# Kernel tuning notes

Measured on AMD Instinct MI355X. Metric: run time of the kernel, lower is better.

Reference implementation:

```python
import jax, jax.numpy as jnp
import numpy as np
from jax import lax

B, L, T = 16, 128, 1024          # batch, phoneme len, mel frames
D, H, F, NL = 384, 2, 1536, 6    # d_model, heads, ffn dim, layers per stack
V, NMEL, CDP = 128, 80, 256      # vocab, mel bins, duration-predictor channels
NEG = -1e9

def make_posenc(max_pos, d):
    pos = np.arange(max_pos, dtype=np.float32)[:, None]
    i = np.arange(d, dtype=np.float32)[None, :]
    ang = pos / np.power(10000.0, 2.0 * np.floor(i / 2.0) / d)
    pe = np.zeros((max_pos, d), np.float32)
    pe[:, 0::2] = np.sin(ang[:, 0::2])
    pe[:, 1::2] = np.cos(ang[:, 1::2])
    return jnp.asarray(pe)

POS = make_posenc(T, D)

def layer_norm(x, g, b, eps=1e-6):
    m = jnp.mean(x, -1, keepdims=True)
    v = jnp.mean(jnp.square(x - m), -1, keepdims=True)
    return (x - m) * lax.rsqrt(v + eps) * g + b

def mha(x, wq, bq, wk, bk, wv, bv, wo, bo, mask):
    b, s, d = x.shape
    dh = d // H
    def split(t):
        return t.reshape(b, s, H, dh).transpose(0, 2, 1, 3)  # bhsd
    q, k, v = split(x @ wq + bq), split(x @ wk + bk), split(x @ wv + bv)
    logits = jnp.einsum('bhqd,bhkd->bhqk', q, k) / jnp.sqrt(jnp.float32(dh))
    logits = logits + mask * NEG  # mask: [B,1,1,S], 1.0 = masked (as in source)
    w = jax.nn.softmax(logits, axis=-1)
    o = jnp.einsum('bhqk,bhkd->bhqd', w, v).transpose(0, 2, 1, 3).reshape(b, s, d)
    return o @ wo + bo

def fft_stack(x, mask, aw, ab, w1, b1, w2, b2, lnp):
    for i in range(aw.shape[0]):
        a = mha(x, aw[i, 0], ab[i, 0], aw[i, 1], ab[i, 1], aw[i, 2], ab[i, 2], aw[i, 3], ab[i, 3], mask)
        x = layer_norm(x + a, lnp[i, 0, 0], lnp[i, 0, 1])
        f = jax.nn.relu(x @ w1[i] + b1[i]) @ w2[i] + b2[i]
        x = layer_norm(x + f, lnp[i, 1, 0], lnp[i, 1, 1])
    return x

def conv1d_same(x, w, b):
    # x: [B,S,Cin], w: [K,Cin,Cout]
    return lax.conv_general_dilated(x, w, (1,), 'SAME', dimension_numbers=('NWC', 'WIO', 'NWC')) + b

def setup_inputs() -> dict:
    key = jax.random.key(0)
    ks = iter(jax.random.split(key, 24))
    nrm = lambda shape: jax.random.normal(next(ks), shape, jnp.float32) * 0.02
    ln_init = lambda nl, c: jnp.broadcast_to(jnp.stack([jnp.ones(c, jnp.float32), jnp.zeros(c, jnp.float32)]), (nl, 2, 2, c))
    inp = {
        'phonemes': jax.random.randint(next(ks), (B, L), 1, V, jnp.int32),
        'durations': jax.random.randint(next(ks), (B, L), 1, 16, jnp.int32),
        'embed': nrm((V, D)),
        'alpha_enc': jnp.float32(1.0),
        'alpha_dec': jnp.float32(1.0),
        'enc_attn_w': nrm((NL, 4, D, D)), 'enc_attn_b': jnp.zeros((NL, 4, D), jnp.float32),
        'enc_ffn_w1': nrm((NL, D, F)), 'enc_ffn_b1': jnp.zeros((NL, F), jnp.float32),
        'enc_ffn_w2': nrm((NL, F, D)), 'enc_ffn_b2': jnp.zeros((NL, D), jnp.float32),
        'enc_ln': ln_init(NL, D),
        'dec_attn_w': nrm((NL, 4, D, D)), 'dec_attn_b': jnp.zeros((NL, 4, D), jnp.float32),
        'dec_ffn_w1': nrm((NL, D, F)), 'dec_ffn_b1': jnp.zeros((NL, F), jnp.float32),
        'dec_ffn_w2': nrm((NL, F, D)), 'dec_ffn_b2': jnp.zeros((NL, D), jnp.float32),
        'dec_ln': ln_init(NL, D),
        'dp_conv1_w': nrm((3, D, CDP)), 'dp_conv1_b': jnp.zeros((CDP,), jnp.float32),
        'dp_conv2_w': nrm((3, CDP, CDP)), 'dp_conv2_b': jnp.zeros((CDP,), jnp.float32),
        'dp_ln': jnp.broadcast_to(jnp.stack([jnp.ones(CDP, jnp.float32), jnp.zeros(CDP, jnp.float32)]), (2, 2, CDP)),
        'dp_out_w': nrm((CDP, 1)), 'dp_out_b': jnp.zeros((1,), jnp.float32),
        'mel_w': nrm((D, NMEL)), 'mel_b': jnp.zeros((NMEL,), jnp.float32),
    }
    return inp

def reference(phonemes, durations, embed, alpha_enc, alpha_dec,
              enc_attn_w, enc_attn_b, enc_ffn_w1, enc_ffn_b1, enc_ffn_w2, enc_ffn_b2, enc_ln,
              dec_attn_w, dec_attn_b, dec_ffn_w1, dec_ffn_b1, dec_ffn_w2, dec_ffn_b2, dec_ln,
              dp_conv1_w, dp_conv1_b, dp_conv2_w, dp_conv2_b, dp_ln, dp_out_w, dp_out_b,
              mel_w, mel_b):
    Lp = phonemes.shape[1]
    # phoneme encoder with scaled positional encoding
    x = embed[phonemes] + alpha_enc * POS[None, :Lp, :]
    enc_mask = (phonemes == 0).astype(jnp.float32)[:, None, None, :]
    h = fft_stack(x, enc_mask, enc_attn_w, enc_attn_b, enc_ffn_w1, enc_ffn_b1, enc_ffn_w2, enc_ffn_b2, enc_ln)
    # duration predictor: conv1d -> relu -> LN, x2, then linear (log durations)
    d1 = layer_norm(jax.nn.relu(conv1d_same(h, dp_conv1_w, dp_conv1_b)), dp_ln[0, 0], dp_ln[0, 1])
    d2 = layer_norm(jax.nn.relu(conv1d_same(d1, dp_conv2_w, dp_conv2_b)), dp_ln[1, 0], dp_ln[1, 1])
    dur_pred = (d2 @ dp_out_w + dp_out_b)[..., 0]  # [B, L]
    # length regulator: expand each phoneme state by its (teacher) duration via gather
    cum = jnp.cumsum(durations, axis=1)  # [B, L]
    frames = jnp.arange(T)
    idx = jax.vmap(lambda c: jnp.searchsorted(c, frames, side='right'))(cum)  # [B, T]
    idx = jnp.clip(idx, 0, Lp - 1)
    y = jnp.take_along_axis(h, idx[:, :, None], axis=1)  # [B, T, D]
    valid = (frames[None, :] < cum[:, -1:]).astype(jnp.float32)  # [B, T]
    y = y * valid[:, :, None]
    # mel decoder
    y = y + alpha_dec * POS[None, :T, :]
    dec_mask = (1.0 - valid)[:, None, None, :]
    m = fft_stack(y, dec_mask, dec_attn_w, dec_attn_b, dec_ffn_w1, dec_ffn_b1, dec_ffn_w2, dec_ffn_b2, dec_ln)
    mel = m @ mel_w + mel_b  # [B, T, NMEL]
    return mel, dur_pred
```

## Files before the change

### kernel.cpp

```cpp
#include <hip/hip_runtime.h>
#include <math.h>

#define BATCH 16
#define LPH 128
#define TFR 1024
#define DMODEL 384
#define FDIM 1536
#define NLAYER 6
#define NMELB 80
#define CDPC 256
#define NEGV (-1e9f)

typedef unsigned short u16;
typedef __attribute__((ext_vector_type(8))) short short8;
typedef __attribute__((ext_vector_type(4))) float f32x4;

__device__ __forceinline__ float b2f(u16 u) {
  return __uint_as_float(((unsigned)u) << 16);
}
__device__ __forceinline__ u16 f2b(float f) {
  unsigned x = __float_as_uint(f);
  return (u16)((x + 0x7fffu + ((x >> 16) & 1u)) >> 16);
}
__device__ __forceinline__ unsigned cvtpk(float lo, float hi) {
  unsigned r;
  asm volatile("v_cvt_pk_bf16_f32 %0, %1, %2" : "=v"(r) : "v"(lo), "v"(hi));
  return r;
}

#define GLOAD16(gp, lp)                                                                   \
  __builtin_amdgcn_global_load_lds((const __attribute__((address_space(1))) void*)(gp),   \
                                   (__attribute__((address_space(3))) void*)(lp), 16, 0, 0)

#define FBIAS 1
#define FRES 2
#define FRELU 4
#define FOB16 8
#define FVT 16

template <int FL>
__global__ __launch_bounds__(256) void bgemm(
    const u16* __restrict__ A, const u16* __restrict__ Bt,
    const float* __restrict__ bias, const float* __restrict__ res,
    void* __restrict__ Cv, u16* __restrict__ VtP,
    int N, int K, int lda, int ldb, int ldc,
    int zdiv, long az0, long az1, long bz0, long bz1, long cz0, long cz1, int S) {
  constexpr int SMEMSZ = (FL & FVT) ? (128 * 136) : 8192;
  __shared__ __align__(16) u16 smem[SMEMSZ];
  u16* As = smem;
  u16* Bs = smem + 4096;
  const int tid = threadIdx.x;
  const int wave = tid >> 6, lane = tid & 63;
  const int wm = wave >> 1, wn = wave & 1;
  const int lrow = lane & 15, lk = lane >> 4;
  const int z = blockIdx.z;
  const int zq = z / zdiv, zr = z - zq * zdiv;
  const long offA = (long)zq * az0 + (long)zr * az1;
  const long offB = (long)zq * bz0 + (long)zr * bz1;
  const long offC = (long)zq * cz0 + (long)zr * cz1;
  const int fid = blockIdx.x + gridDim.x * blockIdx.y;
  const int idx = fid >> 3;
  const int xl = idx % gridDim.x;
  const int yl = (fid & 7) + 8 * (idx / gridDim.x);
  const int row0 = yl * 128;
  const int col0 = xl * 128;

  const int sj = wave * 2;
  const int srow = lane >> 2;
  const int skc = (lane & 3) * 8;
  const u16* gA = A + offA + (long)(row0 + sj * 16 + srow) * lda + skc;
  const u16* gB = Bt + offB + (long)(col0 + sj * 16 + srow) * ldb + skc;
  u16* lA = As + sj * 512;
  u16* lB = Bs + sj * 512;
  const long ldak = 16L * lda;
  const long ldbk = 16L * ldb;

  f32x4 acc[4][4];
  const f32x4 zero4 = {0.f, 0.f, 0.f, 0.f};
#pragma unroll
  for (int i = 0; i < 4; i++)
#pragma unroll
    for (int j = 0; j < 4; j++) acc[i][j] = zero4;

  const int aoff = (wm * 64 + lrow) * 32 + lk * 8;
  const int boff = (wn * 64 + lrow) * 32 + lk * 8;

  for (int k0 = 0; k0 < K; k0 += 32) {
    GLOAD16(gA, lA);
    GLOAD16(gA + ldak, lA + 512);
    GLOAD16(gB, lB);
    GLOAD16(gB + ldbk, lB + 512);
    gA += 32; gB += 32;
    __syncthreads();
    short8 av[4], bv[4];
#pragma unroll
    for (int mi = 0; mi < 4; mi++) av[mi] = *(const short8*)&As[aoff + mi * 512];
#pragma unroll
    for (int ni = 0; ni < 4; ni++) bv[ni] = *(const short8*)&Bs[boff + ni * 512];
#pragma unroll
    for (int mi = 0; mi < 4; mi++)
#pragma unroll
      for (int ni = 0; ni < 4; ni++)
        acc[mi][ni] = __builtin_amdgcn_mfma_f32_16x16x32_bf16(av[mi], bv[ni], acc[mi][ni], 0, 0, 0);
    __syncthreads();
  }

  const float* bz = (FL & FBIAS) ? bias + (long)z * N : nullptr;
  if constexpr ((FL & FVT) != 0) {
    if (z == 2) {
      u16* Ts = smem;
#pragma unroll
      for (int mi = 0; mi < 4; mi++) {
        int si = wm * 64 + lk * 4 + mi * 16;
#pragma unroll
        for (int ni = 0; ni < 4; ni++) {
          int cl = wn * 64 + ni * 16 + lrow;
          float bi = bz[col0 + cl];
          ushort4 o;
          o.x = f2b(acc[mi][ni][0] + bi);
          o.y = f2b(acc[mi][ni][1] + bi);
          o.z = f2b(acc[mi][ni][2] + bi);
          o.w = f2b(acc[mi][ni][3] + bi);
          *(ushort4*)&Ts[cl * 136 + si] = o;
        }
      }
      __syncthreads();
      const int ci = tid >> 1;
      const int cbase = (tid & 1) * 64;
      int c = col0 + ci;
      int hh = c / 192, dd = c - hh * 192;
      int bb = row0 / S;
      int ss = row0 % S;
      u16* dst = &VtP[((long)(bb * 2 + hh) * 256 + dd) * S + ss + cbase];
      const u16* srcr = &Ts[ci * 136 + cbase];
#pragma unroll
      for (int j = 0; j < 8; j++)
        *(short8*)&dst[j * 8] = *(const short8*)&srcr[j * 8];
      return;
    }
  }
  float* Cf = (float*)Cv + offC;
  u16* Cb = (u16*)Cv + offC;
  const float* resz = (FL & FRES) ? res + offC : nullptr;
#pragma unroll
  for (int mi = 0; mi < 4; mi++) {
    long rbase = row0 + wm * 64 + lk * 4 + (long)mi * 16;
#pragma unroll
    for (int ni = 0; ni < 4; ni++) {
      int c = col0 + wn * 64 + ni * 16 + lrow;
      if (c < N) {
        float bi = (FL & FBIAS) ? bz[c] : 0.f;
#pragma unroll
        for (int rr = 0; rr < 4; rr++) {
          float vv = acc[mi][ni][rr] + bi;
          if (FL & FRES) vv += resz[(rbase + rr) * (long)ldc + c];
          if (FL & FRELU) vv = fmaxf(vv, 0.f);
          if (FL & FOB16) Cb[(rbase + rr) * (long)ldc + c] = f2b(vv);
          else Cf[(rbase + rr) * (long)ldc + c] = vv;
        }
      }
    }
  }
}

#define KSW(r, c) ((r) * 192 + ((c) ^ (((r)&7) << 3)))
#define VSTR 40
#define PSTR 40
__global__ __launch_bounds__(512) void fattn(const u16* __restrict__ qb, const u16* __restrict__ kb,
                                             const u16* __restrict__ vt,
                                             const float* __restrict__ maska,
                                             u16* __restrict__ opart, float* __restrict__ mlpart,
                                             int S, int qtshift) {
  __shared__ __align__(16) u16 Ks[32 * 192];
  __shared__ __align__(16) u16 Vs[192 * VSTR];
  __shared__ __align__(16) u16 PsT[8][16 * PSTR];
  const int tid = threadIdx.x;
  const int w = tid >> 6, l = tid & 63;
  const int g = l >> 4, lr = l & 15;
  const int QT = gridDim.x;
  const int fid = (blockIdx.z * 32 + blockIdx.y) * QT + blockIdx.x;
  const int s = fid >> 3;
  const int gid = (fid & 7) * 8 + (s >> qtshift);
  const int qt = s & (QT - 1);
  const int bh = gid & 31, z = gid >> 5;
  const int b = bh >> 1, h = bh & 1;
  const int q0 = qt * 128 + w * 16;
  const int hoff = h * 192;
  const int KS = S >> 1;
  const int kbeg = z * KS;
  const float scale = 0.0721687836f;

  const int k0r = tid / 24, k0c = (tid % 24) * 8;
  const bool c1K = (tid < 256);
  const int c1i = c1K ? (tid + 512) : (tid - 256);
  const int k1r = c1i / 24, k1c = (c1i % 24) * 8;
  const int v1r = c1i >> 2, v1c = (c1i & 3) * 8;
  const int v2 = tid + 256;
  const int v2r = v2 >> 2, v2c = (v2 & 3) * 8;
  const u16* kbase = kb + (long)b * S * 384 + hoff;
  const u16* vbase = vt + (long)bh * 256 * S;

  const long qrowb = ((long)b * S + q0 + lr) * 384 + hoff + g * 8;
  short8 qf[6];
#pragma unroll
  for (int ks = 0; ks < 6; ks++) qf[ks] = *(const short8*)&qb[qrowb + ks * 32];

  f32x4 accO[12];
  const f32x4 zero4 = {0.f, 0.f, 0.f, 0.f};
#pragma unroll
  for (int j = 0; j < 12; j++) accO[j] = zero4;
  float m = -1e30f, lsum = 0.f;

  short8 st0, st1, st2;
  st0 = *(const short8*)&kbase[(long)(kbeg + k0r) * 384 + k0c];
  st1 = c1K ? *(const short8*)&kbase[(long)(kbeg + k1r) * 384 + k1c]
            : *(const short8*)&vbase[(long)v1r * S + kbeg + v1c];
  st2 = *(const short8*)&vbase[(long)v2r * S + kbeg + v2c];

  for (int kt = kbeg; kt < kbeg + KS; kt += 32) {
    __syncthreads();
    *(short8*)&Ks[KSW(k0r, k0c)] = st0;
    if (c1K) *(short8*)&Ks[KSW(k1r, k1c)] = st1;
    else *(short8*)&Vs[v1r * VSTR + v1c] = st1;
    *(short8*)&Vs[v2r * VSTR + v2c] = st2;
    __syncthreads();
    if (kt + 32 < kbeg + KS) {
      st0 = *(const short8*)&kbase[(long)(kt + 32 + k0r) * 384 + k0c];
      st1 = c1K ? *(const short8*)&kbase[(long)(kt + 32 + k1r) * 384 + k1c]
                : *(const short8*)&vbase[(long)v1r * S + kt + 32 + v1c];
      st2 = *(const short8*)&vbase[(long)v2r * S + kt + 32 + v2c];
    }
    f32x4 sa0 = zero4, sb0 = zero4, sa1 = zero4, sb1 = zero4;
    __builtin_amdgcn_s_setprio(1);
#pragma unroll
    for (int ks = 0; ks < 3; ks++) {
      short8 k0 = *(const short8*)&Ks[KSW(lr, ks * 32 + g * 8)];
      short8 k1 = *(const short8*)&Ks[KSW(16 + lr, ks * 32 + g * 8)];
      sa0 = __builtin_amdgcn_mfma_f32_16x16x32_bf16(k0, qf[ks], sa0, 0, 0, 0);
      sa1 = __builtin_amdgcn_mfma_f32_16x16x32_bf16(k1, qf[ks], sa1, 0, 0, 0);
    }
#pragma unroll
    for (int ks = 3; ks < 6; ks++) {
      short8 k0 = *(const short8*)&Ks[KSW(lr, ks * 32 + g * 8)];
      short8 k1 = *(const short8*)&Ks[KSW(16 + lr, ks * 32 + g * 8)];
      sb0 = __builtin_amdgcn_mfma_f32_16x16x32_bf16(k0, qf[ks], sb0, 0, 0, 0);
      sb1 = __builtin_amdgcn_mfma_f32_16x16x32_bf16(k1, qf[ks], sb1, 0, 0, 0);
    }
    __builtin_amdgcn_s_setprio(0);
    f32x4 sacc[2];
    sacc[0] = sa0 + sb0;
    sacc[1] = sa1 + sb1;
#pragma unroll
    for (int f = 0; f < 2; f++) {
      if (maska) {
        float4 mk4 = *(const float4*)&maska[(long)b * S + kt + f * 16 + 4 * g];
        sacc[f][0] = fmaf(sacc[f][0], scale, mk4.x);
        sacc[f][1] = fmaf(sacc[f][1], scale, mk4.y);
        sacc[f][2] = fmaf(sacc[f][2], scale, mk4.z);
        sacc[f][3] = fmaf(sacc[f][3], scale, mk4.w);
      } else {
#pragma unroll
        for (int r = 0; r < 4; r++) sacc[f][r] *= scale;
      }
    }
    float tm = sacc[0][0];
#pragma unroll
    for (int r = 1; r < 4; r++) tm = fmaxf(tm, sacc[0][r]);
#pragma unroll
    for (int r = 0; r < 4; r++) tm = fmaxf(tm, sacc[1][r]);
    tm = fmaxf(tm, __shfl_xor(tm, 16));
    tm = fmaxf(tm, __shfl_xor(tm, 32));
    if (__any(tm > m + 8.f)) {
      float mn = fmaxf(m, tm);
      float al = __expf(m - mn);
      m = mn;
      lsum *= al;
#pragma unroll
      for (int j = 0; j < 12; j++)
#pragma unroll
        for (int r = 0; r < 4; r++) accO[j][r] *= al;
    }
    float rs = 0.f;
#pragma unroll
    for (int f = 0; f < 2; f++)
#pragma unroll
      for (int r = 0; r < 4; r++) {
        float p = __expf(sacc[f][r] - m);
        sacc[f][r] = p;
        rs += p;
      }
    rs += __shfl_xor(rs, 16);
    rs += __shfl_xor(rs, 32);
    lsum += rs;
#pragma unroll
    for (int f = 0; f < 2; f++) {
      uint2 pp;
      pp.x = cvtpk(sacc[f][0], sacc[f][1]);
      pp.y = cvtpk(sacc[f][2], sacc[f][3]);
      *(uint2*)&PsT[w][lr * PSTR + f * 16 + 4 * g] = pp;
    }
    {
      short8 pT = *(const short8*)&PsT[w][lr * PSTR + g * 8];
      __builtin_amdgcn_s_setprio(1);
#pragma unroll
      for (int j = 0; j < 12; j++) {
        short8 vf = *(const short8*)&Vs[(j * 16 + lr) * VSTR + g * 8];
        accO[j] = __builtin_amdgcn_mfma_f32_16x16x32_bf16(vf, pT, accO[j], 0, 0, 0);
      }
      __builtin_amdgcn_s_setprio(0);
    }
  }
  const long orow = ((long)(z * 32 + bh) * S + q0 + lr) * 192;
#pragma unroll
  for (int j = 0; j < 12; j++) {
    uint2 oo;
    oo.x = cvtpk(accO[j][0], accO[j][1]);
    oo.y = cvtpk(accO[j][2], accO[j][3]);
    *(uint2*)&opart[orow + j * 16 + 4 * g] = oo;
  }
  if (g == 0) {
    long mi = ((long)(z * 32 + bh) * S + q0 + lr) * 2;
    mlpart[mi] = m;
    mlpart[mi + 1] = lsum;
  }
}

__global__ __launch_bounds__(256) void fmerge(const u16* __restrict__ opart,
                                              const float* __restrict__ mlpart,
                                              u16* __restrict__ ob, int S) {
  long cid = (long)blockIdx.x * 256 + threadIdx.x;
  long nch = (long)32 * S * 24;
  if (cid >= nch) return;
  int row = (int)(cid / 24);
  int c8 = (int)(cid % 24) * 8;
  int bh = row / S, q = row - bh * S;
  int b = bh >> 1, h = bh & 1;
  long zs = (long)32 * S;
  float m0 = mlpart[(long)row * 2], l0 = mlpart[(long)row * 2 + 1];
  float m1 = mlpart[(zs + row) * 2], l1 = mlpart[(zs + row) * 2 + 1];
  float M = fmaxf(m0, m1);
  float a0 = __expf(m0 - M), a1 = __expf(m1 - M);
  float invL = 1.f / (a0 * l0 + a1 * l1);
  a0 *= invL; a1 *= invL;
  short8 o0 = *(const short8*)&opart[(long)row * 192 + c8];
  short8 o1 = *(const short8*)&opart[zs * 192 + (long)row * 192 + c8];
  float v[8];
#pragma unroll
  for (int j = 0; j < 8; j++)
    v[j] = a0 * b2f((u16)o0[j]) + a1 * b2f((u16)o1[j]);
  uint4 oo;
  oo.x = cvtpk(v[0], v[1]);
  oo.y = cvtpk(v[2], v[3]);
  oo.z = cvtpk(v[4], v[5]);
  oo.w = cvtpk(v[6], v[7]);
  *(uint4*)&ob[((long)b * S + q) * 384 + h * 192 + c8] = oo;
}

__global__ void wconv_t(const float* __restrict__ src, u16* __restrict__ dst, int K, int N) {
  __shared__ float t[32][33];
  long mb = blockIdx.z;
  src += mb * (long)K * N;
  dst += mb * (long)K * N;
  int n0 = blockIdx.x * 32, k0 = blockIdx.y * 32;
  int tx = threadIdx.x, ty = threadIdx.y;
#pragma unroll
  for (int i = 0; i < 4; i++) {
    int r = ty + i * 8;
    t[r][tx] = src[(long)(k0 + r) * N + n0 + tx];
  }
  __syncthreads();
#pragma unroll
  for (int i = 0; i < 4; i++) {
    int r = ty + i * 8;
    dst[(long)(n0 + r) * K + k0 + tx] = f2b(t[tx][r]);
  }
}

__global__ void melw_t(const float* __restrict__ src, u16* __restrict__ dst) {
  int i = blockIdx.x * 256 + threadIdx.x;
  if (i >= 128 * 384) return;
  int n = i / 384, kk2 = i - n * 384;
  dst[i] = (n < NMELB) ? f2b(src[(long)kk2 * NMELB + n]) : (u16)0;
}

__global__ void posenc_kernel(float* __restrict__ pe) {
  int i = blockIdx.x * 256 + threadIdx.x;
  if (i >= TFR * DMODEL) return;
  int t = i / DMODEL, d = i - t * DMODEL;
  float f = (2.0f * (float)(d >> 1)) / (float)DMODEL;
  float ang = (float)t * powf(10000.0f, -f);
  pe[i] = (d & 1) ? cosf(ang) : sinf(ang);
}

__global__ void embed_kernel(const int* __restrict__ ph, const float* __restrict__ emb,
                             const float* __restrict__ pe, const float* __restrict__ alpha,
                             float* __restrict__ x, u16* __restrict__ xb) {
  int i = blockIdx.x * 256 + threadIdx.x;
  if (i >= BATCH * LPH * DMODEL) return;
  int d = i % DMODEL;
  int bl = i / DMODEL;
  int l = bl % LPH;
  float v = emb[ph[bl] * DMODEL + d] + alpha[0] * pe[l * DMODEL + d];
  x[i] = v;
  xb[i] = f2b(v);
}

template <int C>
__global__ __launch_bounds__(256) void lnw(float* __restrict__ x, const float* __restrict__ gamma,
                                           const float* __restrict__ beta,
                                           float* __restrict__ outf, u16* __restrict__ outb) {
  const int w = threadIdx.x >> 6, l = threadIdx.x & 63;
  const long row = (long)blockIdx.x * 4 + w;
  float* xr = x + row * C;
  float v[C / 64];
  float s1 = 0.f, s2 = 0.f;
#pragma unroll
  for (int i = 0; i < C / 64; i++) {
    v[i] = xr[l + i * 64];
    s1 += v[i];
    s2 += v[i] * v[i];
  }
#pragma unroll
  for (int off = 1; off < 64; off <<= 1) {
    s1 += __shfl_xor(s1, off);
    s2 += __shfl_xor(s2, off);
  }
  float mean = s1 / C;
  float var = s2 / C - mean * mean;
  float rstd = rsqrtf(var + 1e-6f);
  float* tf = outf ? outf + row * C : xr;
#pragma unroll
  for (int i = 0; i < C / 64; i++) {
    float o = (v[i] - mean) * rstd * gamma[l + i * 64] + beta[l + i * 64];
    tf[l + i * 64] = o;
    if (outb) outb[row * C + l + i * 64] = f2b(o);
  }
}

template <int C>
__global__ __launch_bounds__(256) void lnsum(const u16* __restrict__ p0, const u16* __restrict__ p1,
                                             const float* __restrict__ bias,
                                             float* __restrict__ x, const float* __restrict__ gamma,
                                             const float* __restrict__ beta,
                                             float* __restrict__ outf, u16* __restrict__ outb) {
  const int w = threadIdx.x >> 6, l = threadIdx.x & 63;
  const long row = (long)blockIdx.x * 4 + w;
  float* xr = x + row * C;
  float v[C / 64];
  float s1 = 0.f, s2 = 0.f;
#pragma unroll
  for (int i = 0; i < C / 64; i++) {
    int c = l + i * 64;
    v[i] = b2f(p0[row * C + c]) + b2f(p1[row * C + c]) + bias[c] + xr[c];
    s1 += v[i];
    s2 += v[i] * v[i];
  }
#pragma unroll
  for (int off = 1; off < 64; off <<= 1) {
    s1 += __shfl_xor(s1, off);
    s2 += __shfl_xor(s2, off);
  }
  float mean = s1 / C;
  float var = s2 / C - mean * mean;
  float rstd = rsqrtf(var + 1e-6f);
  float* tf = outf ? outf + row * C : xr;
#pragma unroll
  for (int i = 0; i < C / 64; i++) {
    int c = l + i * 64;
    float o = (v[i] - mean) * rstd * gamma[c] + beta[c];
    tf[c] = o;
    if (outb) outb[row * C + c] = f2b(o);
  }
}

template <int CIN>
__global__ __launch_bounds__(256) void im2col3(const float* __restrict__ x,
                                               u16* __restrict__ a) {
  const int PER = (3 * CIN) / 8;
  long idx = (long)blockIdx.x * 256 + threadIdx.x;
  if (idx >= (long)BATCH * LPH * PER) return;
  int row = (int)(idx / PER);
  int e8 = (int)(idx - (long)row * PER) * 8;
  int kk = e8 / CIN, ci = e8 - kk * CIN;
  int b = row >> 7, l = row & (LPH - 1);
  int gl = l + kk - 1;
  ushort4 o0 = {0, 0, 0, 0}, o1 = {0, 0, 0, 0};
  if (gl >= 0 && gl < LPH) {
    const float* src = x + ((long)(b * LPH + gl) * CIN + ci);
    float4 v0 = *(const float4*)src;
    float4 v1 = *(const float4*)(src + 4);
    o0.x = f2b(v0.x); o0.y = f2b(v0.y); o0.z = f2b(v0.z); o0.w = f2b(v0.w);
    o1.x = f2b(v1.x); o1.y = f2b(v1.y); o1.z = f2b(v1.z); o1.w = f2b(v1.w);
  }
  *(ushort4*)&a[(long)row * (3 * CIN) + e8] = o0;
  *(ushort4*)&a[(long)row * (3 * CIN) + e8 + 4] = o1;
}

__global__ void dpout_kernel(const float* __restrict__ d2, const float* __restrict__ w,
                             const float* __restrict__ bb, float* __restrict__ out) {
  int wv = threadIdx.x >> 6, lane = threadIdx.x & 63;
  int row = blockIdx.x * 4 + wv;
  const float* xr = d2 + (long)row * CDPC;
  float s = 0.f;
  for (int c = lane; c < CDPC; c += 64) s = fmaf(xr[c], w[c], s);
#pragma unroll
  for (int off = 32; off > 0; off >>= 1) s += __shfl_down(s, off);
  if (lane == 0) out[row] = s + bb[0];
}

__global__ void regulator_kernel(const int* __restrict__ durations, int* __restrict__ idx,
                                 float* __restrict__ maskv, float* __restrict__ maska) {
  __shared__ int cum[LPH];
  __shared__ int total;
  int b = blockIdx.x;
  if (threadIdx.x == 0) {
    int s = 0;
    for (int j = 0; j < LPH; j++) { s += durations[b * LPH + j]; cum[j] = s; }
    total = s;
  }
  __syncthreads();
  for (int t = threadIdx.x; t < TFR; t += blockDim.x) {
    int cnt = 0;
    for (int j = 0; j < LPH; j++) cnt += (cum[j] <= t) ? 1 : 0;
    if (cnt > LPH - 1) cnt = LPH - 1;
    idx[b * TFR + t] = cnt;
    maskv[b * TFR + t] = (t < total) ? 0.f : 1.f;
    maska[b * TFR + t] = (t < total) ? 0.f : NEGV;
  }
}

__global__ void gather_kernel(const float* __restrict__ h, const int* __restrict__ idx,
                              const float* __restrict__ maskv, const float* __restrict__ pe,
                              const float* __restrict__ alpha, float* __restrict__ y,
                              u16* __restrict__ yb) {
  long i = (long)blockIdx.x * 256 + threadIdx.x;
  if (i >= (long)BATCH * TFR * DMODEL) return;
  int d = (int)(i % DMODEL);
  long bt = i / DMODEL;
  int t = (int)(bt % TFR);
  long b = bt / TFR;
  float valid = 1.0f - maskv[bt];
  float v = h[((long)b * LPH + idx[bt]) * DMODEL + d] * valid + alpha[0] * pe[t * DMODEL + d];
  y[i] = v;
  yb[i] = f2b(v);
}

extern "C" void kernel_launch(void* const* d_in, const int* in_sizes, int n_in,
                              void* d_out, int out_size, void* d_ws, size_t ws_size,
                              hipStream_t stream) {
  const int* phonemes = (const int*)d_in[0];
  const int* durations = (const int*)d_in[1];
  const float* embedw = (const float*)d_in[2];
  const float* alpha_enc = (const float*)d_in[3];
  const float* alpha_dec = (const float*)d_in[4];
  const float* enc_attn_w = (const float*)d_in[5];
  const float* enc_attn_b = (const float*)d_in[6];
  const float* enc_ffn_w1 = (const float*)d_in[7];
  const float* enc_ffn_b1 = (const float*)d_in[8];
  const float* enc_ffn_w2 = (const float*)d_in[9];
  const float* enc_ffn_b2 = (const float*)d_in[10];
  const float* enc_ln = (const float*)d_in[11];
  const float* dec_attn_w = (const float*)d_in[12];
  const float* dec_attn_b = (const float*)d_in[13];
  const float* dec_ffn_w1 = (const float*)d_in[14];
  const float* dec_ffn_b1 = (const float*)d_in[15];
  const float* dec_ffn_w2 = (const float*)d_in[16];
  const float* dec_ffn_b2 = (const float*)d_in[17];
  const float* dec_ln = (const float*)d_in[18];
  const float* dp_conv1_w = (const float*)d_in[19];
  const float* dp_conv1_b = (const float*)d_in[20];
  const float* dp_conv2_w = (const float*)d_in[21];
  const float* dp_conv2_b = (const float*)d_in[22];
  const float* dp_ln = (const float*)d_in[23];
  const float* dp_out_w = (const float*)d_in[24];
  const float* dp_out_b = (const float*)d_in[25];
  const float* mel_w = (const float*)d_in[26];
  const float* mel_b = (const float*)d_in[27];

  char* base = (char*)d_ws;
  float* X0 = (float*)base;
  u16* Xb = (u16*)(base + 25165824);
  u16* QKb = (u16*)(base + 37748736);
  char* E = base + 62914560;
  u16* Vt = (u16*)(base + 96468992);
  u16* Wb = (u16*)(base + 113246208);
  float* Henc = (float*)(base + 134479872);
  float* PE = (float*)(base + 137625600);
  float* MASKD = (float*)(base + 139198464);
  int* IDX = (int*)(base + 139264000);
  u16* Wmel = (u16*)(base + 139329536);
  float* MASKA = (float*)(base + 139427840);

  u16* AOb = QKb;
  u16* Mb = QKb;

  u16* OPART = (u16*)E;
  float* MLPART = (float*)(E + 25165824);

  u16* AOP = (u16*)E;
  const long FFN2OFF = (96468992L - 25165824L) / 2;

  float* DP1 = (float*)E;
  float* DP2 = DP1 + (size_t)2048 * CDPC;
  u16* A1 = (u16*)(E + 4 * 1024 * 1024);
  u16* A2 = (u16*)(E + 9 * 1024 * 1024);
  u16* Wdp1 = (u16*)(E + 13 * 1024 * 1024);
  u16* Wdp2 = (u16*)(E + 15 * 1024 * 1024);

  u16* WAt = Wb;
  u16* W1t = Wb + 3538944;
  u16* W2t = Wb + 7077888;

  const int Me = BATCH * LPH;
  const int Md = BATCH * TFR;
  const long DD = 384L * 384;
  const long NXe = (long)Me * DMODEL;
  const long NXd = (long)Md * DMODEL;
  dim3 tb32(32, 8);

  posenc_kernel<<<(TFR * DMODEL + 255) / 256, 256, 0, stream>>>(PE);
  embed_kernel<<<(Me * DMODEL + 255) / 256, 256, 0, stream>>>(phonemes, embedw, PE, alpha_enc,
                                                              X0, Xb);
  wconv_t<<<dim3(12, 12, 24), tb32, 0, stream>>>(enc_attn_w, WAt, 384, 384);
  wconv_t<<<dim3(48, 12, 6), tb32, 0, stream>>>(enc_ffn_w1, W1t, 384, 1536);
  wconv_t<<<dim3(12, 48, 6), tb32, 0, stream>>>(enc_ffn_w2, W2t, 1536, 384);
  melw_t<<<192, 256, 0, stream>>>(mel_w, Wmel);

  for (int i = 0; i < NLAYER; i++) {
    const u16* wa = WAt + (size_t)i * 4 * DD;
    const float* ab = enc_attn_b + (size_t)i * 4 * 384;
    bgemm<(FBIAS | FOB16 | FVT)><<<dim3(3, 16, 3), 256, 0, stream>>>(
        Xb, wa, ab, nullptr, QKb, Vt, 384, 384, 384, 384, 384,
        1, 0, 0, DD, 0, NXe, 0, 128);
    fattn<<<dim3(1, 32, 2), 512, 0, stream>>>(QKb, QKb + NXe, Vt, nullptr, OPART, MLPART, 128, 0);
    fmerge<<<384, 256, 0, stream>>>(OPART, MLPART, AOb, 128);
    bgemm<(FOB16)><<<dim3(3, 16, 2), 256, 0, stream>>>(
        AOb, wa + 3 * DD, nullptr, nullptr, AOP, nullptr, 384, 192, 384, 384, 384,
        2, 0, 192, 0, 192, 0, NXe, 0);
    lnsum<384><<<Me / 4, 256, 0, stream>>>(AOP, AOP + NXe, ab + 3 * 384, X0,
                                           enc_ln + ((size_t)(i * 2 + 0) * 2 + 0) * 384,
                                           enc_ln + ((size_t)(i * 2 + 0) * 2 + 1) * 384,
                                           nullptr, Xb);
    bgemm<(FBIAS | FRELU | FOB16)><<<dim3(12, 16, 1), 256, 0, stream>>>(
        Xb, W1t + (size_t)i * 589824, enc_ffn_b1 + (size_t)i * 1536, nullptr, Mb, nullptr,
        1536, 384, 384, 384, 1536, 1, 0, 0, 0, 0, 0, 0, 0);
    bgemm<(FOB16)><<<dim3(3, 16, 2), 256, 0, stream>>>(
        Mb, W2t + (size_t)i * 589824, nullptr, nullptr, Xb, nullptr,
        384, 768, 1536, 1536, 384, 2, 0, 768, 0, 768, 0, FFN2OFF, 0);
    lnsum<384><<<Me / 4, 256, 0, stream>>>(Xb, Xb + FFN2OFF, enc_ffn_b2 + (size_t)i * 384, X0,
                                           enc_ln + ((size_t)(i * 2 + 1) * 2 + 0) * 384,
                                           enc_ln + ((size_t)(i * 2 + 1) * 2 + 1) * 384,
                                           (i == NLAYER - 1) ? Henc : nullptr,
                                           (i == NLAYER - 1) ? nullptr : Xb);
  }

  wconv_t<<<dim3(8, 36, 1), tb32, 0, stream>>>(dp_conv1_w, Wdp1, 1152, 256);
  wconv_t<<<dim3(8, 24, 1), tb32, 0, stream>>>(dp_conv2_w, Wdp2, 768, 256);
  im2col3<DMODEL><<<(Me * 144 + 255) / 256, 256, 0, stream>>>(Henc, A1);
  bgemm<(FBIAS | FRELU)><<<dim3(2, 16, 1), 256, 0, stream>>>(
      A1, Wdp1, dp_conv1_b, nullptr, DP1, nullptr, 256, 1152, 1152, 1152, 256,
      1, 0, 0, 0, 0, 0, 0, 0);
  lnw<256><<<Me / 4, 256, 0, stream>>>(DP1, dp_ln + 0 * CDPC, dp_ln + 1 * CDPC, nullptr, nullptr);
  im2col3<CDPC><<<(Me * 96 + 255) / 256, 256, 0, stream>>>(DP1, A2);
  bgemm<(FBIAS | FRELU)><<<dim3(2, 16, 1), 256, 0, stream>>>(
      A2, Wdp2, dp_conv2_b, nullptr, DP2, nullptr, 256, 768, 768, 768, 256,
      1, 0, 0, 0, 0, 0, 0, 0);
  lnw<256><<<Me / 4, 256, 0, stream>>>(DP2, dp_ln + 2 * CDPC, dp_ln + 3 * CDPC, nullptr, nullptr);
  float* durout = (float*)d_out + (size_t)Md * NMELB;
  dpout_kernel<<<Me / 4, 256, 0, stream>>>(DP2, dp_out_w, dp_out_b, durout);

  regulator_kernel<<<BATCH, 256, 0, stream>>>(durations, IDX, MASKD, MASKA);
  gather_kernel<<<(int)((NXd + 255) / 256), 256, 0, stream>>>(Henc, IDX, MASKD, PE, alpha_dec,
                                                              X0, Xb);
  wconv_t<<<dim3(12, 12, 24), tb32, 0, stream>>>(dec_attn_w, WAt, 384, 384);
  wconv_t<<<dim3(48, 12, 6), tb32, 0, stream>>>(dec_ffn_w1, W1t, 384, 1536);
  wconv_t<<<dim3(12, 48, 6), tb32, 0, stream>>>(dec_ffn_w2, W2t, 1536, 384);

  for (int i = 0; i < NLAYER; i++) {
    const u16* wa = WAt + (size_t)i * 4 * DD;
    const float* ab = dec_attn_b + (size_t)i * 4 * 384;
    bgemm<(FBIAS | FOB16 | FVT)><<<dim3(3, 128, 3), 256, 0, stream>>>(
        Xb, wa, ab, nullptr, QKb, Vt, 384, 384, 384, 384, 384,
        1, 0, 0, DD, 0, NXd, 0, 1024);
    fattn<<<dim3(8, 32, 2), 512, 0, stream>>>(QKb, QKb + NXd, Vt, MASKA, OPART, MLPART, 1024, 3);
    fmerge<<<3072, 256, 0, stream>>>(OPART, MLPART, AOb, 1024);
    bgemm<(FOB16)><<<dim3(3, 128, 2), 256, 0, stream>>>(
        AOb, wa + 3 * DD, nullptr, nullptr, AOP, nullptr, 384, 192, 384, 384, 384,
        2, 0, 192, 0, 192, 0, NXd, 0);
    lnsum<384><<<Md / 4, 256, 0, stream>>>(AOP, AOP + NXd, ab + 3 * 384, X0,
                                           dec_ln + ((size_t)(i * 2 + 0) * 2 + 0) * 384,
                                           dec_ln + ((size_t)(i * 2 + 0) * 2 + 1) * 384,
                                           nullptr, Xb);
    bgemm<(FBIAS | FRELU | FOB16)><<<dim3(12, 128, 1), 256, 0, stream>>>(
        Xb, W1t + (size_t)i * 589824, dec_ffn_b1 + (size_t)i * 1536, nullptr, Mb, nullptr,
        1536, 384, 384, 384, 1536, 1, 0, 0, 0, 0, 0, 0, 0);
    bgemm<(FOB16)><<<dim3(3, 128, 2), 256, 0, stream>>>(
        Mb, W2t + (size_t)i * 589824, nullptr, nullptr, Xb, nullptr,
        384, 768, 1536, 1536, 384, 2, 0, 768, 0, 768, 0, FFN2OFF, 0);
    lnsum<384><<<Md / 4, 256, 0, stream>>>(Xb, Xb + FFN2OFF, dec_ffn_b2 + (size_t)i * 384, X0,
                                           dec_ln + ((size_t)(i * 2 + 1) * 2 + 0) * 384,
                                           dec_ln + ((size_t)(i * 2 + 1) * 2 + 1) * 384,
                                           nullptr, Xb);
  }

  bgemm<(FBIAS)><<<dim3(1, 128, 1), 256, 0, stream>>>(
      Xb, Wmel, mel_b, nullptr, (float*)d_out, nullptr, 80, 384, 384, 384, 80,
      1, 0, 0, 0, 0, 0, 0, 0);
}
```

Baseline: 1.953 ms.

## Widen attention key tile to 64 and drop fp32 residual stream

The flash-attention kernel now stages 64 keys per iteration instead of 32, with wider V and P shared-memory strides and a launch-bounds occupancy hint. This halves the number of barriers and loop iterations and gives more MFMA work per sync. Separately, the fp32 residual copy X0 is removed and the residual is read from the bf16 activation buffer. The FFN split-K partial outputs move into the freed region. This cuts residual-stream memory traffic but adds bf16 rounding to the residual path, and the larger tile raises shared-memory and register pressure.

```diff
diff --git a/kernel.cpp b/kernel.cpp
--- a/kernel.cpp
+++ b/kernel.cpp
@@ -164,14 +164,16 @@
 }
 
 #define KSW(r, c) ((r) * 192 + ((c) ^ (((r)&7) << 3)))
-#define VSTR 40
-#define PSTR 40
-__global__ __launch_bounds__(512) void fattn(const u16* __restrict__ qb, const u16* __restrict__ kb,
-                                             const u16* __restrict__ vt,
-                                             const float* __restrict__ maska,
-                                             u16* __restrict__ opart, float* __restrict__ mlpart,
-                                             int S, int qtshift) {
-  __shared__ __align__(16) u16 Ks[32 * 192];
+#define VSTR 72
+#define PSTR 72
+__global__ __launch_bounds__(512, 4) void fattn(const u16* __restrict__ qb,
+                                                const u16* __restrict__ kb,
+                                                const u16* __restrict__ vt,
+                                                const float* __restrict__ maska,
+                                                u16* __restrict__ opart,
+                                                float* __restrict__ mlpart,
+                                                int S, int qtshift) {
+  __shared__ __align__(16) u16 Ks[64 * 192];
   __shared__ __align__(16) u16 Vs[192 * VSTR];
   __shared__ __align__(16) u16 PsT[8][16 * PSTR];
   const int tid = threadIdx.x;
@@ -190,13 +192,13 @@
   const int kbeg = z * KS;
   const float scale = 0.0721687836f;
 
-  const int k0r = tid / 24, k0c = (tid % 24) * 8;
-  const bool c1K = (tid < 256);
-  const int c1i = c1K ? (tid + 512) : (tid - 256);
-  const int k1r = c1i / 24, k1c = (c1i % 24) * 8;
-  const int v1r = c1i >> 2, v1c = (c1i & 3) * 8;
-  const int v2 = tid + 256;
-  const int v2r = v2 >> 2, v2c = (v2 & 3) * 8;
+  int kr[3], kc[3], vr[3], vc[3];
+#pragma unroll
+  for (int i = 0; i < 3; i++) {
+    int c = tid + i * 512;
+    kr[i] = c / 24; kc[i] = (c % 24) * 8;
+    vr[i] = c >> 3; vc[i] = (c & 7) * 8;
+  }
   const u16* kbase = kb + (long)b * S * 384 + hoff;
   const u16* vbase = vt + (long)bh * 256 * S;
 
@@ -211,47 +213,43 @@
   for (int j = 0; j < 12; j++) accO[j] = zero4;
   float m = -1e30f, lsum = 0.f;
 
-  short8 st0, st1, st2;
-  st0 = *(const short8*)&kbase[(long)(kbeg + k0r) * 384 + k0c];
-  st1 = c1K ? *(const short8*)&kbase[(long)(kbeg + k1r) * 384 + k1c]
-            : *(const short8*)&vbase[(long)v1r * S + kbeg + v1c];
-  st2 = *(const short8*)&vbase[(long)v2r * S + kbeg + v2c];
-
-  for (int kt = kbeg; kt < kbeg + KS; kt += 32) {
+  short8 kst[3], vst[3];
+#pragma unroll
+  for (int i = 0; i < 3; i++) {
+    kst[i] = *(const short8*)&kbase[(long)(kbeg + kr[i]) * 384 + kc[i]];
+    vst[i] = *(const short8*)&vbase[(long)vr[i] * S + kbeg + vc[i]];
+  }
+
+  for (int kt = kbeg; kt < kbeg + KS; kt += 64) {
     __syncthreads();
-    *(short8*)&Ks[KSW(k0r, k0c)] = st0;
-    if (c1K) *(short8*)&Ks[KSW(k1r, k1c)] = st1;
-    else *(short8*)&Vs[v1r * VSTR + v1c] = st1;
-    *(short8*)&Vs[v2r * VSTR + v2c] = st2;
+#pragma unroll
+    for (int i = 0; i < 3; i++) {
+      *(short8*)&Ks[KSW(kr[i], kc[i])] = kst[i];
+      *(short8*)&Vs[vr[i] * VSTR + vc[i]] = vst[i];
+    }
     __syncthreads();
-    if (kt + 32 < kbeg + KS) {
-      st0 = *(const short8*)&kbase[(long)(kt + 32 + k0r) * 384 + k0c];
-      st1 = c1K ? *(const short8*)&kbase[(long)(kt + 32 + k1r) * 384 + k1c]
-                : *(const short8*)&vbase[(long)v1r * S + kt + 32 + v1c];
-      st2 = *(const short8*)&vbase[(long)v2r * S + kt + 32 + v2c];
-    }
-    f32x4 sa0 = zero4, sb0 = zero4, sa1 = zero4, sb1 = zero4;
+    if (kt + 64 < kbeg + KS) {
+#pragma unroll
+      for (int i = 0; i < 3; i++) {
+        kst[i] = *(const short8*)&kbase[(long)(kt + 64 + kr[i]) * 384 + kc[i]];
+        vst[i] = *(const short8*)&vbase[(long)vr[i] * S + kt + 64 + vc[i]];
+      }
+    }
+    f32x4 sacc[4];
+#pragma unroll
+    for (int f = 0; f < 4; f++) sacc[f] = zero4;
     __builtin_amdgcn_s_setprio(1);
 #pragma unroll
-    for (int ks = 0; ks < 3; ks++) {
-      short8 k0 = *(const short8*)&Ks[KSW(lr, ks * 32 + g * 8)];
-      short8 k1 = *(const short8*)&Ks[KSW(16 + lr, ks * 32 + g * 8)];
-      sa0 = __builtin_amdgcn_mfma_f32_16x16x32_bf16(k0, qf[ks], sa0, 0, 0, 0);
-      sa1 = __builtin_amdgcn_mfma_f32_16x16x32_bf16(k1, qf[ks], sa1, 0, 0, 0);
-    }
-#pragma unroll
-    for (int ks = 3; ks < 6; ks++) {
-      short8 k0 = *(const short8*)&Ks[KSW(lr, ks * 32 + g * 8)];
-      short8 k1 = *(const short8*)&Ks[KSW(16 + lr, ks * 32 + g * 8)];
-      sb0 = __builtin_amdgcn_mfma_f32_16x16x32_bf16(k0, qf[ks], sb0, 0, 0, 0);
-      sb1 = __builtin_amdgcn_mfma_f32_16x16x32_bf16(k1, qf[ks], sb1, 0, 0, 0);
+    for (int ks = 0; ks < 6; ks++) {
+#pragma unroll
+      for (int f = 0; f < 4; f++) {
+        short8 kf = *(const short8*)&Ks[KSW(f * 16 + lr, ks * 32 + g * 8)];
+        sacc[f] = __builtin_amdgcn_mfma_f32_16x16x32_bf16(kf, qf[ks], sacc[f], 0, 0, 0);
+      }
     }
     __builtin_amdgcn_s_setprio(0);
-    f32x4 sacc[2];
-    sacc[0] = sa0 + sb0;
-    sacc[1] = sa1 + sb1;
-#pragma unroll
-    for (int f = 0; f < 2; f++) {
+#pragma unroll
+    for (int f = 0; f < 4; f++) {
       if (maska) {
         float4 mk4 = *(const float4*)&maska[(long)b * S + kt + f * 16 + 4 * g];
         sacc[f][0] = fmaf(sacc[f][0], scale, mk4.x);
@@ -265,9 +263,9 @@
     }
     float tm = sacc[0][0];
 #pragma unroll
-    for (int r = 1; r < 4; r++) tm = fmaxf(tm, sacc[0][r]);
-#pragma unroll
-    for (int r = 0; r < 4; r++) tm = fmaxf(tm, sacc[1][r]);
+    for (int f = 0; f < 4; f++)
+#pragma unroll
+      for (int r = 0; r < 4; r++) tm = fmaxf(tm, sacc[f][r]);
     tm = fmaxf(tm, __shfl_xor(tm, 16));
     tm = fmaxf(tm, __shfl_xor(tm, 32));
     if (__any(tm > m + 8.f)) {
@@ -282,7 +280,7 @@
     }
     float rs = 0.f;
 #pragma unroll
-    for (int f = 0; f < 2; f++)
+    for (int f = 0; f < 4; f++)
 #pragma unroll
       for (int r = 0; r < 4; r++) {
         float p = __expf(sacc[f][r] - m);
@@ -293,22 +291,23 @@
     rs += __shfl_xor(rs, 32);
     lsum += rs;
 #pragma unroll
-    for (int f = 0; f < 2; f++) {
+    for (int f = 0; f < 4; f++) {
       uint2 pp;
       pp.x = cvtpk(sacc[f][0], sacc[f][1]);
       pp.y = cvtpk(sacc[f][2], sacc[f][3]);
       *(uint2*)&PsT[w][lr * PSTR + f * 16 + 4 * g] = pp;
     }
-    {
-      short8 pT = *(const short8*)&PsT[w][lr * PSTR + g * 8];
-      __builtin_amdgcn_s_setprio(1);
+    __builtin_amdgcn_s_setprio(1);
+#pragma unroll
+    for (int ks = 0; ks < 2; ks++) {
+      short8 pT = *(const short8*)&PsT[w][lr * PSTR + ks * 32 + g * 8];
 #pragma unroll
       for (int j = 0; j < 12; j++) {
-        short8 vf = *(const short8*)&Vs[(j * 16 + lr) * VSTR + g * 8];
+        short8 vf = *(const short8*)&Vs[(j * 16 + lr) * VSTR + ks * 32 + g * 8];
         accO[j] = __builtin_amdgcn_mfma_f32_16x16x32_bf16(vf, pT, accO[j], 0, 0, 0);
       }
-      __builtin_amdgcn_s_setprio(0);
-    }
+    }
+    __builtin_amdgcn_s_setprio(0);
   }
   const long orow = ((long)(z * 32 + bh) * S + q0 + lr) * 192;
 #pragma unroll
@@ -394,14 +393,13 @@
 
 __global__ void embed_kernel(const int* __restrict__ ph, const float* __restrict__ emb,
                              const float* __restrict__ pe, const float* __restrict__ alpha,
-                             float* __restrict__ x, u16* __restrict__ xb) {
+                             u16* __restrict__ xb) {
   int i = blockIdx.x * 256 + threadIdx.x;
   if (i >= BATCH * LPH * DMODEL) return;
   int d = i % DMODEL;
   int bl = i / DMODEL;
   int l = bl % LPH;
   float v = emb[ph[bl] * DMODEL + d] + alpha[0] * pe[l * DMODEL + d];
-  x[i] = v;
   xb[i] = f2b(v);
 }
 
@@ -440,18 +438,18 @@
 template <int C>
 __global__ __launch_bounds__(256) void lnsum(const u16* __restrict__ p0, const u16* __restrict__ p1,
                                              const float* __restrict__ bias,
-                                             float* __restrict__ x, const float* __restrict__ gamma,
+                                             const u16* __restrict__ resb,
+                                             const float* __restrict__ gamma,
                                              const float* __restrict__ beta,
                                              float* __restrict__ outf, u16* __restrict__ outb) {
   const int w = threadIdx.x >> 6, l = threadIdx.x & 63;
   const long row = (long)blockIdx.x * 4 + w;
-  float* xr = x + row * C;
   float v[C / 64];
   float s1 = 0.f, s2 = 0.f;
 #pragma unroll
   for (int i = 0; i < C / 64; i++) {
     int c = l + i * 64;
-    v[i] = b2f(p0[row * C + c]) + b2f(p1[row * C + c]) + bias[c] + xr[c];
+    v[i] = b2f(p0[row * C + c]) + b2f(p1[row * C + c]) + bias[c] + b2f(resb[row * C + c]);
     s1 += v[i];
     s2 += v[i] * v[i];
   }
@@ -463,12 +461,11 @@
   float mean = s1 / C;
   float var = s2 / C - mean * mean;
   float rstd = rsqrtf(var + 1e-6f);
-  float* tf = outf ? outf + row * C : xr;
 #pragma unroll
   for (int i = 0; i < C / 64; i++) {
     int c = l + i * 64;
     float o = (v[i] - mean) * rstd * gamma[c] + beta[c];
-    tf[c] = o;
+    if (outf) outf[row * C + c] = o;
     if (outb) outb[row * C + c] = f2b(o);
   }
 }
@@ -531,8 +528,7 @@
 
 __global__ void gather_kernel(const float* __restrict__ h, const int* __restrict__ idx,
                               const float* __restrict__ maskv, const float* __restrict__ pe,
-                              const float* __restrict__ alpha, float* __restrict__ y,
-                              u16* __restrict__ yb) {
+                              const float* __restrict__ alpha, u16* __restrict__ yb) {
   long i = (long)blockIdx.x * 256 + threadIdx.x;
   if (i >= (long)BATCH * TFR * DMODEL) return;
   int d = (int)(i % DMODEL);
@@ -541,7 +537,6 @@
   long b = bt / TFR;
   float valid = 1.0f - maskv[bt];
   float v = h[((long)b * LPH + idx[bt]) * DMODEL + d] * valid + alpha[0] * pe[t * DMODEL + d];
-  y[i] = v;
   yb[i] = f2b(v);
 }
 
@@ -578,7 +573,7 @@
   const float* mel_b = (const float*)d_in[27];
 
   char* base = (char*)d_ws;
-  float* X0 = (float*)base;
+  u16* FP = (u16*)base;
   u16* Xb = (u16*)(base + 25165824);
   u16* QKb = (u16*)(base + 37748736);
   char* E = base + 62914560;
@@ -596,9 +591,7 @@
 
   u16* OPART = (u16*)E;
   float* MLPART = (float*)(E + 25165824);
-
   u16* AOP = (u16*)E;
-  const long FFN2OFF = (96468992L - 25165824L) / 2;
 
   float* DP1 = (float*)E;
   float* DP2 = DP1 + (size_t)2048 * CDPC;
@@ -619,8 +612,7 @@
   dim3 tb32(32, 8);
 
   posenc_kernel<<<(TFR * DMODEL + 255) / 256, 256, 0, stream>>>(PE);
-  embed_kernel<<<(Me * DMODEL + 255) / 256, 256, 0, stream>>>(phonemes, embedw, PE, alpha_enc,
-                                                              X0, Xb);
+  embed_kernel<<<(Me * DMODEL + 255) / 256, 256, 0, stream>>>(phonemes, embedw, PE, alpha_enc, Xb);
   wconv_t<<<dim3(12, 12, 24), tb32, 0, stream>>>(enc_attn_w, WAt, 384, 384);
   wconv_t<<<dim3(48, 12, 6), tb32, 0, stream>>>(enc_ffn_w1, W1t, 384, 1536);
   wconv_t<<<dim3(12, 48, 6), tb32, 0, stream>>>(enc_ffn_w2, W2t, 1536, 384);
@@ -637,7 +629,7 @@
     bgemm<(FOB16)><<<dim3(3, 16, 2), 256, 0, stream>>>(
         AOb, wa + 3 * DD, nullptr, nullptr, AOP, nullptr, 384, 192, 384, 384, 384,
         2, 0, 192, 0, 192, 0, NXe, 0);
-    lnsum<384><<<Me / 4, 256, 0, stream>>>(AOP, AOP + NXe, ab + 3 * 384, X0,
+    lnsum<384><<<Me / 4, 256, 0, stream>>>(AOP, AOP + NXe, ab + 3 * 384, Xb,
                                            enc_ln + ((size_t)(i * 2 + 0) * 2 + 0) * 384,
                                            enc_ln + ((size_t)(i * 2 + 0) * 2 + 1) * 384,
                                            nullptr, Xb);
@@ -645,13 +637,12 @@
         Xb, W1t + (size_t)i * 589824, enc_ffn_b1 + (size_t)i * 1536, nullptr, Mb, nullptr,
         1536, 384, 384, 384, 1536, 1, 0, 0, 0, 0, 0, 0, 0);
     bgemm<(FOB16)><<<dim3(3, 16, 2), 256, 0, stream>>>(
-        Mb, W2t + (size_t)i * 589824, nullptr, nullptr, Xb, nullptr,
-        384, 768, 1536, 1536, 384, 2, 0, 768, 0, 768, 0, FFN2OFF, 0);
-    lnsum<384><<<Me / 4, 256, 0, stream>>>(Xb, Xb + FFN2OFF, enc_ffn_b2 + (size_t)i * 384, X0,
+        Mb, W2t + (size_t)i * 589824, nullptr, nullptr, FP, nullptr,
+        384, 768, 1536, 1536, 384, 2, 0, 768, 0, 768, 0, NXe, 0);
+    lnsum<384><<<Me / 4, 256, 0, stream>>>(FP, FP + NXe, enc_ffn_b2 + (size_t)i * 384, Xb,
                                            enc_ln + ((size_t)(i * 2 + 1) * 2 + 0) * 384,
                                            enc_ln + ((size_t)(i * 2 + 1) * 2 + 1) * 384,
-                                           (i == NLAYER - 1) ? Henc : nullptr,
-                                           (i == NLAYER - 1) ? nullptr : Xb);
+                                           (i == NLAYER - 1) ? Henc : nullptr, Xb);
   }
 
   wconv_t<<<dim3(8, 36, 1), tb32, 0, stream>>>(dp_conv1_w, Wdp1, 1152, 256);
@@ -670,8 +661,7 @@
   dpout_kernel<<<Me / 4, 256, 0, stream>>>(DP2, dp_out_w, dp_out_b, durout);
 
   regulator_kernel<<<BATCH, 256, 0, stream>>>(durations, IDX, MASKD, MASKA);
-  gather_kernel<<<(int)((NXd + 255) / 256), 256, 0, stream>>>(Henc, IDX, MASKD, PE, alpha_dec,
-                                                              X0, Xb);
+  gather_kernel<<<(int)((NXd + 255) / 256), 256, 0, stream>>>(Henc, IDX, MASKD, PE, alpha_dec, Xb);
   wconv_t<<<dim3(12, 12, 24), tb32, 0, stream>>>(dec_attn_w, WAt, 384, 384);
   wconv_t<<<dim3(48, 12, 6), tb32, 0, stream>>>(dec_ffn_w1, W1t, 384, 1536);
   wconv_t<<<dim3(12, 48, 6), tb32, 0, stream>>>(dec_ffn_w2, W2t, 1536, 384);
@@ -687,7 +677,7 @@
     bgemm<(FOB16)><<<dim3(3, 128, 2), 256, 0, stream>>>(
         AOb, wa + 3 * DD, nullptr, nullptr, AOP, nullptr, 384, 192, 384, 384, 384,
         2, 0, 192, 0, 192, 0, NXd, 0);
-    lnsum<384><<<Md / 4, 256, 0, stream>>>(AOP, AOP + NXd, ab + 3 * 384, X0,
+    lnsum<384><<<Md / 4, 256, 0, stream>>>(AOP, AOP + NXd, ab + 3 * 384, Xb,
                                            dec_ln + ((size_t)(i * 2 + 0) * 2 + 0) * 384,
                                            dec_ln + ((size_t)(i * 2 + 0) * 2 + 1) * 384,
                                            nullptr, Xb);
@@ -695,9 +685,9 @@
         Xb, W1t + (size_t)i * 589824, dec_ffn_b1 + (size_t)i * 1536, nullptr, Mb, nullptr,
         1536, 384, 384, 384, 1536, 1, 0, 0, 0, 0, 0, 0, 0);
     bgemm<(FOB16)><<<dim3(3, 128, 2), 256, 0, stream>>>(
-        Mb, W2t + (size_t)i * 589824, nullptr, nullptr, Xb, nullptr,
-        384, 768, 1536, 1536, 384, 2, 0, 768, 0, 768, 0, FFN2OFF, 0);
-    lnsum<384><<<Md / 4, 256, 0, stream>>>(Xb, Xb + FFN2OFF, dec_ffn_b2 + (size_t)i * 384, X0,
+        Mb, W2t + (size_t)i * 589824, nullptr, nullptr, FP, nullptr,
+        384, 768, 1536, 1536, 384, 2, 0, 768, 0, 768, 0, NXd, 0);
+    lnsum<384><<<Md / 4, 256, 0, stream>>>(FP, FP + NXd, dec_ffn_b2 + (size_t)i * 384, Xb,
                                            dec_ln + ((size_t)(i * 2 + 1) * 2 + 0) * 384,
                                            dec_ln + ((size_t)(i * 2 + 1) * 2 + 1) * 384,
                                            nullptr, Xb);
```

After: 2.231 ms. 14.3% more time.
